# Kernel tuning notes

Measured on AMD Instinct MI355X. Metric: run time of the kernel, lower is better.

The kernel has to match this reference:

```python
import jax, jax.numpy as jnp
import numpy as np

N = 50000   # nodes
E = 800000  # edges (avg degree 16)
D = 128     # in_feats == out_feats


def setup_inputs() -> dict:
    key = jax.random.key(0)
    k1, k2, k3, k4 = jax.random.split(key, 4)
    h = jax.random.normal(k1, (N, D), dtype=jnp.float32)
    src = jax.random.randint(k2, (E,), 0, N, dtype=jnp.int32)
    dst = jax.random.randint(k3, (E,), 0, N, dtype=jnp.int32)
    snorm_n = jnp.ones((N, 1), dtype=jnp.float32)  # sqrt(1/N) replicated; identity-scaled here
    # NodeApply linear: Linear(2*D, D) with bias
    W = jax.random.normal(k4, (D, 2 * D), dtype=jnp.float32) / np.sqrt(2 * D).astype(np.float32)
    b = jnp.zeros((D,), dtype=jnp.float32)
    return {"h": h, "snorm_n": snorm_n, "W": W, "b": b, "src": src, "dst": dst}


def reference(h, snorm_n, W, b, src, dst):
    # dropout p=0.0 -> identity
    h_in = h
    # gather neighbor messages and segment-mean aggregate (MeanAggregator)
    ones = jnp.ones((src.shape[0],), dtype=h.dtype)
    deg = jax.ops.segment_sum(ones, dst, num_segments=N)            # [N]
    msg_sum = jax.ops.segment_sum(h[src], dst, num_segments=N)     # [N, D]
    c = msg_sum / jnp.maximum(deg, 1.0)[:, None]                   # zero-degree nodes -> c = 0
    # NodeApply: concat -> linear -> L2 normalize -> relu
    bundle = jnp.concatenate([h, c], axis=1) @ W.T + b             # [N, D]
    nrm = jnp.sqrt(jnp.sum(bundle * bundle, axis=1, keepdims=True))
    bundle = bundle / jnp.maximum(nrm, 1e-12)                      # F.normalize(p=2, dim=1)
    out = jax.nn.relu(bundle)
    # graph norm
    out = out * snorm_n
    # residual (in_feats == out_feats)
    return h_in + out
```

## Files before the change

kernel.cpp:

```cpp
#include <hip/hip_runtime.h>
#include <hip/hip_bf16.h>

#define TPB 256
#define CHUNK_LOG 13
#define CHUNK (1 << CHUNK_LOG)
#define HSTRIDE 12544

typedef __attribute__((ext_vector_type(8))) short bf16x8;
typedef __attribute__((ext_vector_type(4))) float f32x4;
typedef __attribute__((ext_vector_type(2))) float f32x2;

__device__ inline unsigned short f2bf(float f) {
    unsigned u = __float_as_uint(f);
    unsigned r = u + 0x7fffu + ((u >> 16) & 1u);
    return (unsigned short)(r >> 16);
}
__device__ inline float bf2f(unsigned short s) {
    return __uint_as_float(((unsigned)s) << 16);
}

__global__ void k_hist(const int* __restrict__ dst,
                       unsigned* __restrict__ hist32, unsigned char* __restrict__ lrank,
                       int E) {
    __shared__ unsigned lhist[HSTRIDE];
    int b = blockIdx.x;
    for (int i = threadIdx.x; i < HSTRIDE; i += TPB) lhist[i] = 0;
    __syncthreads();
    int e0 = b << CHUNK_LOG;
    int e1 = min(e0 + CHUNK, E);
    for (int e = e0 + (int)threadIdx.x; e < e1; e += TPB) {
        int d = dst[e];
        unsigned sh = (d & 3) * 8;
        unsigned old = atomicAdd(&lhist[d >> 2], 1u << sh);
        lrank[e] = (unsigned char)((old >> sh) & 0xffu);
    }
    __syncthreads();
    for (int i = threadIdx.x; i < HSTRIDE; i += TPB)
        hist32[(size_t)b * HSTRIDE + i] = lhist[i];
}

__launch_bounds__(TPB)
__global__ void k_scan(const unsigned* __restrict__ hist32,
                       unsigned short* __restrict__ cbase,
                       int* __restrict__ bsum, unsigned* ctr,
                       int* __restrict__ offs, int N, int E, int NBH) {
    extern __shared__ unsigned tile[];
    __shared__ int sdata[4];
    __shared__ int sb[TPB];
    __shared__ int wsum[4];
    int NB = gridDim.x;
    int bid = blockIdx.x, tid = threadIdx.x;
    int lane = tid & 63, w = tid >> 6;

    int tileBase = bid * 64;
    int total = NBH * 64;
    for (int i = tid; i < total; i += TPB) {
        int b = i >> 6, c = i & 63;
        tile[i] = hist32[(size_t)b * HSTRIDE + tileBase + c];
    }
    __syncthreads();
    int n = bid * TPB + tid;
    unsigned sh = (tid & 3) * 8;
    int wcol = tid >> 2;
    int run = 0;
    for (int b = 0; b < NBH; ++b) {
        int c = (int)((tile[b * 64 + wcol] >> sh) & 0xffu);
        if (n < N) cbase[(size_t)b * N + n] = (unsigned short)run;
        run += c;
    }
    int dv = (n < N) ? run : 0;

    int s = dv;
    for (int o = 32; o; o >>= 1) s += __shfl_xor(s, o);
    if (lane == 0) sdata[w] = s;
    __syncthreads();
    if (tid == 0) {
        int tot = sdata[0] + sdata[1] + sdata[2] + sdata[3];
        __hip_atomic_store(&bsum[bid], tot, __ATOMIC_RELAXED, __HIP_MEMORY_SCOPE_AGENT);
        __hip_atomic_fetch_add(ctr, 1u, __ATOMIC_RELEASE, __HIP_MEMORY_SCOPE_AGENT);
        while (__hip_atomic_load(ctr, __ATOMIC_ACQUIRE, __HIP_MEMORY_SCOPE_AGENT)
               < (unsigned)NB)
            __builtin_amdgcn_s_sleep(2);
    }
    __syncthreads();

    int v = 0;
    if (tid < NB)
        v = __hip_atomic_load(&bsum[tid], __ATOMIC_RELAXED, __HIP_MEMORY_SCOPE_AGENT);
    int x = v;
    for (int o = 1; o < 64; o <<= 1) { int y = __shfl_up(x, o); if (lane >= o) x += y; }
    if (lane == 63) wsum[w] = x;
    __syncthreads();
    int add = 0;
    for (int k = 0; k < w; ++k) add += wsum[k];
    sb[tid] = add + x - v;
    __syncthreads();
    int base = sb[bid];

    int y2 = dv;
    for (int o = 1; o < 64; o <<= 1) { int z = __shfl_up(y2, o); if (lane >= o) y2 += z; }
    __syncthreads();
    if (lane == 63) wsum[w] = y2;
    __syncthreads();
    int add2 = 0;
    for (int k = 0; k < w; ++k) add2 += wsum[k];
    int ex = base + add2 + y2 - dv;
    if (n < N) offs[n] = ex;
    if (n == N - 1) offs[N] = E;
}

__global__ void k_scatterconv(const float* __restrict__ h, const float* __restrict__ W,
                              const int* __restrict__ src, const int* __restrict__ dst,
                              const unsigned char* __restrict__ lrank,
                              const unsigned short* __restrict__ cbase,
                              const int* __restrict__ offs,
                              unsigned short* __restrict__ esrc,
                              unsigned short* __restrict__ h_hi,
                              unsigned* __restrict__ h8,
                              unsigned short* __restrict__ Wb,
                              int N, int E, int nchunk) {
    int nh4 = N * 32;
    int totalc = nh4 + 8192;
    for (int t = blockIdx.x * TPB + threadIdx.x; t < totalc; t += gridDim.x * TPB) {
        if (t < nh4) {
            float4 v = ((const float4*)h)[t];
            ushort4 hi;
            hi.x = f2bf(v.x); hi.y = f2bf(v.y);
            hi.z = f2bf(v.z); hi.w = f2bf(v.w);
            ((ushort4*)h_hi)[t] = hi;
            int p8 = __builtin_amdgcn_cvt_pk_fp8_f32(v.x, v.y, 0, false);
            p8 = __builtin_amdgcn_cvt_pk_fp8_f32(v.z, v.w, p8, true);
            h8[t] = (unsigned)p8;
        } else {
            int w4 = t - nh4;
            float4 v = ((const float4*)W)[w4];
            ushort4 hi;
            hi.x = f2bf(v.x); hi.y = f2bf(v.y);
            hi.z = f2bf(v.z); hi.w = f2bf(v.w);
            ((ushort4*)Wb)[w4] = hi;
        }
    }
    int slice = blockIdx.x & 7;
    int chunk = blockIdx.x >> 3;
    int lo = (int)((long long)N * slice >> 3);
    int hi = (int)((long long)N * (slice + 1) >> 3);
    for (int e = chunk * TPB + threadIdx.x; e < E; e += nchunk * TPB) {
        int d = dst[e];
        if (d >= lo && d < hi) {
            int b = e >> CHUNK_LOG;
            int pos = offs[d] + (int)cbase[(size_t)b * N + d] + (int)lrank[e];
            esrc[pos] = (unsigned short)src[e];
        }
    }
}

__global__ void k_agg(const unsigned* __restrict__ h8, const int* __restrict__ offs,
                      const unsigned short* __restrict__ esrc,
                      unsigned* __restrict__ c, int N) {
    int wav = (blockIdx.x * TPB + threadIdx.x) >> 6;
    int half = (threadIdx.x >> 5) & 1;
    int hl = threadIdx.x & 31;
    int n = wav * 2 + half;
    if (n >= N) return;
    int beg = offs[n], end = offs[n + 1];
    float a0 = 0.f, a1 = 0.f, a2 = 0.f, a3 = 0.f;
    int e = beg;
    for (; e + 3 < end; e += 4) {
        int s0 = esrc[e], s1 = esrc[e + 1], s2 = esrc[e + 2], s3 = esrc[e + 3];
        unsigned u0 = h8[(size_t)s0 * 32 + hl];
        unsigned u1 = h8[(size_t)s1 * 32 + hl];
        unsigned u2 = h8[(size_t)s2 * 32 + hl];
        unsigned u3 = h8[(size_t)s3 * 32 + hl];
        f32x2 p0 = __builtin_amdgcn_cvt_pk_f32_fp8((int)u0, false);
        f32x2 q0 = __builtin_amdgcn_cvt_pk_f32_fp8((int)u0, true);
        f32x2 p1 = __builtin_amdgcn_cvt_pk_f32_fp8((int)u1, false);
        f32x2 q1 = __builtin_amdgcn_cvt_pk_f32_fp8((int)u1, true);
        f32x2 p2 = __builtin_amdgcn_cvt_pk_f32_fp8((int)u2, false);
        f32x2 q2 = __builtin_amdgcn_cvt_pk_f32_fp8((int)u2, true);
        f32x2 p3 = __builtin_amdgcn_cvt_pk_f32_fp8((int)u3, false);
        f32x2 q3 = __builtin_amdgcn_cvt_pk_f32_fp8((int)u3, true);
        a0 += p0.x + p1.x + p2.x + p3.x;
        a1 += p0.y + p1.y + p2.y + p3.y;
        a2 += q0.x + q1.x + q2.x + q3.x;
        a3 += q0.y + q1.y + q2.y + q3.y;
    }
    for (; e < end; ++e) {
        unsigned u0 = h8[(size_t)esrc[e] * 32 + hl];
        f32x2 p0 = __builtin_amdgcn_cvt_pk_f32_fp8((int)u0, false);
        f32x2 q0 = __builtin_amdgcn_cvt_pk_f32_fp8((int)u0, true);
        a0 += p0.x; a1 += p0.y; a2 += q0.x; a3 += q0.y;
    }
    float inv = 1.0f / fmaxf((float)(end - beg), 1.0f);
    unsigned pk0 = ((unsigned)f2bf(a1 * inv) << 16) | (unsigned)f2bf(a0 * inv);
    unsigned pk1 = ((unsigned)f2bf(a3 * inv) << 16) | (unsigned)f2bf(a2 * inv);
    c[(size_t)n * 64 + hl * 2]     = pk0;
    c[(size_t)n * 64 + hl * 2 + 1] = pk1;
}

__launch_bounds__(TPB)
__global__ void k_apply(const unsigned short* __restrict__ h_hi,
                        const unsigned short* __restrict__ c,
                        const unsigned short* __restrict__ Wb,
                        const float* __restrict__ bia,
                        const float* __restrict__ snorm,
                        float* __restrict__ out, int N) {
    int lane = threadIdx.x & 63;
    int l15 = lane & 15, l4 = lane >> 4;
    int wave = threadIdx.x >> 6;
    int r0 = blockIdx.x * 128 + wave * 32;

    f32x4 acc[2][8] = {};

    #pragma unroll
    for (int kc = 0; kc < 8; ++kc) {
        bf16x8 Bf[8];
        #pragma unroll
        for (int n = 0; n < 8; ++n) {
            Bf[n] = *(const bf16x8*)((const char*)Wb +
                     ((size_t)(n * 16 + l15) * 512 + (size_t)kc * 64 + (size_t)l4 * 16));
        }
        #pragma unroll
        for (int rf = 0; rf < 2; ++rf) {
            int row = r0 + rf * 16 + l15;
            if (row > N - 1) row = N - 1;
            bf16x8 av;
            if (kc < 4) {
                av = *(const bf16x8*)((const char*)h_hi +
                      ((size_t)row * 256 + (size_t)kc * 64 + (size_t)l4 * 16));
            } else {
                av = *(const bf16x8*)((const char*)c +
                      ((size_t)row * 256 + (size_t)(kc - 4) * 64 + (size_t)l4 * 16));
            }
            #pragma unroll
            for (int n = 0; n < 8; ++n)
                acc[rf][n] = __builtin_amdgcn_mfma_f32_16x16x32_bf16(av, Bf[n], acc[rf][n], 0, 0, 0);
        }
    }

    float bn[8];
    #pragma unroll
    for (int n = 0; n < 8; ++n) bn[n] = bia[n * 16 + l15];

    #pragma unroll
    for (int rf = 0; rf < 2; ++rf) {
        float sq[4] = {0.f, 0.f, 0.f, 0.f};
        #pragma unroll
        for (int n = 0; n < 8; ++n) {
            #pragma unroll
            for (int g = 0; g < 4; ++g) {
                acc[rf][n][g] += bn[n];
                sq[g] += acc[rf][n][g] * acc[rf][n][g];
            }
        }
        #pragma unroll
        for (int g = 0; g < 4; ++g) {
            sq[g] += __shfl_xor(sq[g], 1);
            sq[g] += __shfl_xor(sq[g], 2);
            sq[g] += __shfl_xor(sq[g], 4);
            sq[g] += __shfl_xor(sq[g], 8);
        }
        #pragma unroll
        for (int g = 0; g < 4; ++g) {
            int row = r0 + rf * 16 + l4 * 4 + g;
            if (row < N) {
                float invn = 1.0f / fmaxf(sqrtf(sq[g]), 1e-12f);
                float sn = snorm[row];
                #pragma unroll
                for (int n = 0; n < 8; ++n) {
                    int col = n * 16 + l15;
                    float res = bf2f(h_hi[(size_t)row * 128 + col]);
                    out[(size_t)row * 128 + col] =
                        fmaxf(acc[rf][n][g] * invn, 0.f) * sn + res;
                }
            }
        }
    }
}

extern "C" void kernel_launch(void* const* d_in, const int* in_sizes, int n_in,
                              void* d_out, int out_size, void* d_ws, size_t ws_size,
                              hipStream_t stream) {
    const float* h     = (const float*)d_in[0];
    const float* snorm = (const float*)d_in[1];
    const float* W     = (const float*)d_in[2];
    const float* b     = (const float*)d_in[3];
    const int*   src   = (const int*)d_in[4];
    const int*   dst   = (const int*)d_in[5];
    int N = in_sizes[1];
    int E = in_sizes[4];
    float* out = (float*)d_out;

    char* ws = (char*)d_ws;
    size_t off = 0;
    auto alloc = [&](size_t bytes) {
        void* ptr = ws + off;
        off = (off + bytes + 255) & ~(size_t)255;
        return ptr;
    };
    int NB  = (N + TPB - 1) / TPB;
    int NBH = (E + CHUNK - 1) >> CHUNK_LOG;
    int* offs   = (int*)alloc((size_t)(N + 1) * 4);
    int* bsum   = (int*)alloc((size_t)NB * 4);
    unsigned* ctr          = (unsigned*)alloc(256);
    unsigned* hist32       = (unsigned*)alloc((size_t)NBH * HSTRIDE * 4);
    unsigned short* cbase  = (unsigned short*)alloc((size_t)NBH * N * 2);
    unsigned char*  lrank  = (unsigned char*)alloc((size_t)E);
    unsigned short* esrc   = (unsigned short*)alloc((size_t)E * 2);
    unsigned short* h_hi   = (unsigned short*)alloc((size_t)N * 128 * 2);
    unsigned*       h8     = (unsigned*)alloc((size_t)N * 128);
    unsigned short* Wb     = (unsigned short*)alloc((size_t)128 * 256 * 2);
    unsigned* c = hist32;

    hipMemsetAsync(ctr, 0, 4, stream);

    k_hist<<<NBH, TPB, 0, stream>>>(dst, hist32, lrank, E);

    size_t tile_bytes = (size_t)NBH * 64 * 4;
    k_scan<<<NB, TPB, tile_bytes, stream>>>(hist32, cbase, bsum, ctr, offs, N, E, NBH);

    int nchunk = 512;
    k_scatterconv<<<8 * nchunk, TPB, 0, stream>>>(h, W, src, dst, lrank, cbase, offs,
                                                  esrc, h_hi, h8, Wb, N, E, nchunk);

    int aggblk = (N + 7) / 8;
    k_agg<<<aggblk, TPB, 0, stream>>>(h8, offs, esrc, c, N);

    int nblk = (N + 127) / 128;
    k_apply<<<nblk, TPB, 0, stream>>>(h_hi, (const unsigned short*)c, Wb, b, snorm, out, N);
}
```

Baseline: 109.9 us.

## Fuse neighbor aggregation into apply kernel via LDS and drop memset

Merges the aggregation and node-apply kernels. Each 16-row block gathers the fp8 neighbor features using 16 lanes per node with 8-byte loads, stores the mean as bf16 into swizzled LDS, then runs the MFMA linear with each wave owning 32 output columns. Row norms are reduced across waves through shared memory, and outputs use nontemporal stores. The counter reset moves from a memset into k_hist. This removes the global round-trip for c and one launch, but every block now reloads W and gets only 16 rows of MFMA work, so the gather latency is less hidden.

```diff
diff --git a/kernel.cpp b/kernel.cpp
--- a/kernel.cpp
+++ b/kernel.cpp
@@ -21,9 +21,10 @@
 
 __global__ void k_hist(const int* __restrict__ dst,
                        unsigned* __restrict__ hist32, unsigned char* __restrict__ lrank,
-                       int E) {
+                       unsigned* ctr, int E) {
     __shared__ unsigned lhist[HSTRIDE];
     int b = blockIdx.x;
+    if (b == 0 && threadIdx.x == 0) *ctr = 0u;
     for (int i = threadIdx.x; i < HSTRIDE; i += TPB) lhist[i] = 0;
     __syncthreads();
     int e0 = b << CHUNK_LOG;
@@ -154,125 +155,132 @@
     }
 }
 
-__global__ void k_agg(const unsigned* __restrict__ h8, const int* __restrict__ offs,
-                      const unsigned short* __restrict__ esrc,
-                      unsigned* __restrict__ c, int N) {
-    int wav = (blockIdx.x * TPB + threadIdx.x) >> 6;
-    int half = (threadIdx.x >> 5) & 1;
-    int hl = threadIdx.x & 31;
-    int n = wav * 2 + half;
-    if (n >= N) return;
-    int beg = offs[n], end = offs[n + 1];
-    float a0 = 0.f, a1 = 0.f, a2 = 0.f, a3 = 0.f;
-    int e = beg;
-    for (; e + 3 < end; e += 4) {
-        int s0 = esrc[e], s1 = esrc[e + 1], s2 = esrc[e + 2], s3 = esrc[e + 3];
-        unsigned u0 = h8[(size_t)s0 * 32 + hl];
-        unsigned u1 = h8[(size_t)s1 * 32 + hl];
-        unsigned u2 = h8[(size_t)s2 * 32 + hl];
-        unsigned u3 = h8[(size_t)s3 * 32 + hl];
-        f32x2 p0 = __builtin_amdgcn_cvt_pk_f32_fp8((int)u0, false);
-        f32x2 q0 = __builtin_amdgcn_cvt_pk_f32_fp8((int)u0, true);
-        f32x2 p1 = __builtin_amdgcn_cvt_pk_f32_fp8((int)u1, false);
-        f32x2 q1 = __builtin_amdgcn_cvt_pk_f32_fp8((int)u1, true);
-        f32x2 p2 = __builtin_amdgcn_cvt_pk_f32_fp8((int)u2, false);
-        f32x2 q2 = __builtin_amdgcn_cvt_pk_f32_fp8((int)u2, true);
-        f32x2 p3 = __builtin_amdgcn_cvt_pk_f32_fp8((int)u3, false);
-        f32x2 q3 = __builtin_amdgcn_cvt_pk_f32_fp8((int)u3, true);
-        a0 += p0.x + p1.x + p2.x + p3.x;
-        a1 += p0.y + p1.y + p2.y + p3.y;
-        a2 += q0.x + q1.x + q2.x + q3.x;
-        a3 += q0.y + q1.y + q2.y + q3.y;
-    }
-    for (; e < end; ++e) {
-        unsigned u0 = h8[(size_t)esrc[e] * 32 + hl];
-        f32x2 p0 = __builtin_amdgcn_cvt_pk_f32_fp8((int)u0, false);
-        f32x2 q0 = __builtin_amdgcn_cvt_pk_f32_fp8((int)u0, true);
-        a0 += p0.x; a1 += p0.y; a2 += q0.x; a3 += q0.y;
-    }
-    float inv = 1.0f / fmaxf((float)(end - beg), 1.0f);
-    unsigned pk0 = ((unsigned)f2bf(a1 * inv) << 16) | (unsigned)f2bf(a0 * inv);
-    unsigned pk1 = ((unsigned)f2bf(a3 * inv) << 16) | (unsigned)f2bf(a2 * inv);
-    c[(size_t)n * 64 + hl * 2]     = pk0;
-    c[(size_t)n * 64 + hl * 2 + 1] = pk1;
-}
-
 __launch_bounds__(TPB)
-__global__ void k_apply(const unsigned short* __restrict__ h_hi,
-                        const unsigned short* __restrict__ c,
-                        const unsigned short* __restrict__ Wb,
-                        const float* __restrict__ bia,
-                        const float* __restrict__ snorm,
-                        float* __restrict__ out, int N) {
-    int lane = threadIdx.x & 63;
+__global__ void k_aggapply(const unsigned short* __restrict__ h_hi,
+                           const unsigned* __restrict__ h8,
+                           const int* __restrict__ offs,
+                           const unsigned short* __restrict__ esrc,
+                           const unsigned short* __restrict__ Wb,
+                           const float* __restrict__ bia,
+                           const float* __restrict__ snorm,
+                           float* __restrict__ out, int N) {
+    __shared__ unsigned short c_lds[16][128];
+    __shared__ float sqp[16][4];
+    int tid = threadIdx.x;
+    int lane = tid & 63;
     int l15 = lane & 15, l4 = lane >> 4;
-    int wave = threadIdx.x >> 6;
-    int r0 = blockIdx.x * 128 + wave * 32;
-
-    f32x4 acc[2][8] = {};
-
+    int wave = tid >> 6;
+    int nb = blockIdx.x * 16;
+
+    {
+        int r = wave * 4 + l4;
+        int n = nb + r; if (n > N - 1) n = N - 1;
+        int beg = offs[n], end = offs[n + 1];
+        const uint2* hq = (const uint2*)h8;
+        float a[8] = {0.f, 0.f, 0.f, 0.f, 0.f, 0.f, 0.f, 0.f};
+        int e = beg;
+        for (; e + 7 < end; e += 8) {
+            uint2 u0 = hq[(size_t)esrc[e]     * 16 + l15];
+            uint2 u1 = hq[(size_t)esrc[e + 1] * 16 + l15];
+            uint2 u2 = hq[(size_t)esrc[e + 2] * 16 + l15];
+            uint2 u3 = hq[(size_t)esrc[e + 3] * 16 + l15];
+            uint2 u4 = hq[(size_t)esrc[e + 4] * 16 + l15];
+            uint2 u5 = hq[(size_t)esrc[e + 5] * 16 + l15];
+            uint2 u6 = hq[(size_t)esrc[e + 6] * 16 + l15];
+            uint2 u7 = hq[(size_t)esrc[e + 7] * 16 + l15];
+            #pragma unroll
+            for (int j = 0; j < 8; ++j) {
+                unsigned ux = (j == 0 ? u0.x : j == 1 ? u1.x : j == 2 ? u2.x : j == 3 ? u3.x
+                              : j == 4 ? u4.x : j == 5 ? u5.x : j == 6 ? u6.x : u7.x);
+                unsigned uy = (j == 0 ? u0.y : j == 1 ? u1.y : j == 2 ? u2.y : j == 3 ? u3.y
+                              : j == 4 ? u4.y : j == 5 ? u5.y : j == 6 ? u6.y : u7.y);
+                f32x2 p = __builtin_amdgcn_cvt_pk_f32_fp8((int)ux, false);
+                f32x2 q = __builtin_amdgcn_cvt_pk_f32_fp8((int)ux, true);
+                f32x2 rr = __builtin_amdgcn_cvt_pk_f32_fp8((int)uy, false);
+                f32x2 ss = __builtin_amdgcn_cvt_pk_f32_fp8((int)uy, true);
+                a[0] += p.x; a[1] += p.y; a[2] += q.x; a[3] += q.y;
+                a[4] += rr.x; a[5] += rr.y; a[6] += ss.x; a[7] += ss.y;
+            }
+        }
+        for (; e < end; ++e) {
+            uint2 u0 = hq[(size_t)esrc[e] * 16 + l15];
+            f32x2 p = __builtin_amdgcn_cvt_pk_f32_fp8((int)u0.x, false);
+            f32x2 q = __builtin_amdgcn_cvt_pk_f32_fp8((int)u0.x, true);
+            f32x2 rr = __builtin_amdgcn_cvt_pk_f32_fp8((int)u0.y, false);
+            f32x2 ss = __builtin_amdgcn_cvt_pk_f32_fp8((int)u0.y, true);
+            a[0] += p.x; a[1] += p.y; a[2] += q.x; a[3] += q.y;
+            a[4] += rr.x; a[5] += rr.y; a[6] += ss.x; a[7] += ss.y;
+        }
+        float inv = 1.0f / fmaxf((float)(end - beg), 1.0f);
+        uint4 pk;
+        pk.x = ((unsigned)f2bf(a[1] * inv) << 16) | (unsigned)f2bf(a[0] * inv);
+        pk.y = ((unsigned)f2bf(a[3] * inv) << 16) | (unsigned)f2bf(a[2] * inv);
+        pk.z = ((unsigned)f2bf(a[5] * inv) << 16) | (unsigned)f2bf(a[4] * inv);
+        pk.w = ((unsigned)f2bf(a[7] * inv) << 16) | (unsigned)f2bf(a[6] * inv);
+        int gs = l15 ^ (r & 7);
+        ((uint4*)&c_lds[r][0])[gs] = pk;
+    }
+    __syncthreads();
+
+    int wc = wave * 32;
+    f32x4 acc0 = {}, acc1 = {};
     #pragma unroll
     for (int kc = 0; kc < 8; ++kc) {
-        bf16x8 Bf[8];
+        bf16x8 Bf0 = *(const bf16x8*)((const char*)Wb +
+                      ((size_t)(wc + l15) * 512 + (size_t)kc * 64 + (size_t)l4 * 16));
+        bf16x8 Bf1 = *(const bf16x8*)((const char*)Wb +
+                      ((size_t)(wc + 16 + l15) * 512 + (size_t)kc * 64 + (size_t)l4 * 16));
+        bf16x8 av;
+        if (kc < 4) {
+            int row = nb + l15; if (row > N - 1) row = N - 1;
+            av = *(const bf16x8*)((const char*)h_hi +
+                  ((size_t)row * 256 + (size_t)kc * 64 + (size_t)l4 * 16));
+        } else {
+            int gi = (kc - 4) * 4 + l4;
+            int gs2 = gi ^ (l15 & 7);
+            av = *(const bf16x8*)((const char*)&c_lds[l15][0] + gs2 * 16);
+        }
+        acc0 = __builtin_amdgcn_mfma_f32_16x16x32_bf16(av, Bf0, acc0, 0, 0, 0);
+        acc1 = __builtin_amdgcn_mfma_f32_16x16x32_bf16(av, Bf1, acc1, 0, 0, 0);
+    }
+
+    float bn0 = bia[wc + l15];
+    float bn1 = bia[wc + 16 + l15];
+    float sq[4];
+    #pragma unroll
+    for (int g = 0; g < 4; ++g) {
+        acc0[g] += bn0;
+        acc1[g] += bn1;
+        sq[g] = acc0[g] * acc0[g] + acc1[g] * acc1[g];
+    }
+    #pragma unroll
+    for (int g = 0; g < 4; ++g) {
+        sq[g] += __shfl_xor(sq[g], 1);
+        sq[g] += __shfl_xor(sq[g], 2);
+        sq[g] += __shfl_xor(sq[g], 4);
+        sq[g] += __shfl_xor(sq[g], 8);
+    }
+    if (l15 == 0) {
         #pragma unroll
-        for (int n = 0; n < 8; ++n) {
-            Bf[n] = *(const bf16x8*)((const char*)Wb +
-                     ((size_t)(n * 16 + l15) * 512 + (size_t)kc * 64 + (size_t)l4 * 16));
-        }
-        #pragma unroll
-        for (int rf = 0; rf < 2; ++rf) {
-            int row = r0 + rf * 16 + l15;
-            if (row > N - 1) row = N - 1;
-            bf16x8 av;
-            if (kc < 4) {
-                av = *(const bf16x8*)((const char*)h_hi +
-                      ((size_t)row * 256 + (size_t)kc * 64 + (size_t)l4 * 16));
-            } else {
-                av = *(const bf16x8*)((const char*)c +
-                      ((size_t)row * 256 + (size_t)(kc - 4) * 64 + (size_t)l4 * 16));
-            }
-            #pragma unroll
-            for (int n = 0; n < 8; ++n)
-                acc[rf][n] = __builtin_amdgcn_mfma_f32_16x16x32_bf16(av, Bf[n], acc[rf][n], 0, 0, 0);
-        }
-    }
-
-    float bn[8];
+        for (int g = 0; g < 4; ++g) sqp[l4 * 4 + g][wave] = sq[g];
+    }
+    __syncthreads();
+
     #pragma unroll
-    for (int n = 0; n < 8; ++n) bn[n] = bia[n * 16 + l15];
-
-    #pragma unroll
-    for (int rf = 0; rf < 2; ++rf) {
-        float sq[4] = {0.f, 0.f, 0.f, 0.f};
-        #pragma unroll
-        for (int n = 0; n < 8; ++n) {
-            #pragma unroll
-            for (int g = 0; g < 4; ++g) {
-                acc[rf][n][g] += bn[n];
-                sq[g] += acc[rf][n][g] * acc[rf][n][g];
-            }
-        }
-        #pragma unroll
-        for (int g = 0; g < 4; ++g) {
-            sq[g] += __shfl_xor(sq[g], 1);
-            sq[g] += __shfl_xor(sq[g], 2);
-            sq[g] += __shfl_xor(sq[g], 4);
-            sq[g] += __shfl_xor(sq[g], 8);
-        }
-        #pragma unroll
-        for (int g = 0; g < 4; ++g) {
-            int row = r0 + rf * 16 + l4 * 4 + g;
-            if (row < N) {
-                float invn = 1.0f / fmaxf(sqrtf(sq[g]), 1e-12f);
-                float sn = snorm[row];
-                #pragma unroll
-                for (int n = 0; n < 8; ++n) {
-                    int col = n * 16 + l15;
-                    float res = bf2f(h_hi[(size_t)row * 128 + col]);
-                    out[(size_t)row * 128 + col] =
-                        fmaxf(acc[rf][n][g] * invn, 0.f) * sn + res;
-                }
-            }
+    for (int g = 0; g < 4; ++g) {
+        int r = l4 * 4 + g;
+        int row = nb + r;
+        if (row < N) {
+            float ssum = sqp[r][0] + sqp[r][1] + sqp[r][2] + sqp[r][3];
+            float invn = 1.0f / fmaxf(sqrtf(ssum), 1e-12f);
+            float sn = snorm[row];
+            int col0 = wc + l15, col1 = wc + 16 + l15;
+            float r0 = bf2f(h_hi[(size_t)row * 128 + col0]);
+            float r1 = bf2f(h_hi[(size_t)row * 128 + col1]);
+            float v0 = fmaxf(acc0[g] * invn, 0.f) * sn + r0;
+            float v1 = fmaxf(acc1[g] * invn, 0.f) * sn + r1;
+            __builtin_nontemporal_store(v0, &out[(size_t)row * 128 + col0]);
+            __builtin_nontemporal_store(v1, &out[(size_t)row * 128 + col1]);
         }
     }
 }
@@ -309,11 +317,8 @@
     unsigned short* h_hi   = (unsigned short*)alloc((size_t)N * 128 * 2);
     unsigned*       h8     = (unsigned*)alloc((size_t)N * 128);
     unsigned short* Wb     = (unsigned short*)alloc((size_t)128 * 256 * 2);
-    unsigned* c = hist32;
-
-    hipMemsetAsync(ctr, 0, 4, stream);
-
-    k_hist<<<NBH, TPB, 0, stream>>>(dst, hist32, lrank, E);
+
+    k_hist<<<NBH, TPB, 0, stream>>>(dst, hist32, lrank, ctr, E);
 
     size_t tile_bytes = (size_t)NBH * 64 * 4;
     k_scan<<<NB, TPB, tile_bytes, stream>>>(hist32, cbase, bsum, ctr, offs, N, E, NBH);
@@ -322,9 +327,6 @@
     k_scatterconv<<<8 * nchunk, TPB, 0, stream>>>(h, W, src, dst, lrank, cbase, offs,
                                                   esrc, h_hi, h8, Wb, N, E, nchunk);
 
-    int aggblk = (N + 7) / 8;
-    k_agg<<<aggblk, TPB, 0, stream>>>(h8, offs, esrc, c, N);
-
-    int nblk = (N + 127) / 128;
-    k_apply<<<nblk, TPB, 0, stream>>>(h_hi, (const unsigned short*)c, Wb, b, snorm, out, N);
-}
+    int nblk = (N + 15) / 16;
+    k_aggapply<<<nblk, TPB, 0, stream>>>(h_hi, h8, offs, esrc, Wb, b, snorm, out, N);
+}
```

Result: no change. 108.1 us (-1.6%).
